# Kernel tuning notes

Hardware: AMD Instinct MI355X
Metric: run time of the kernel (lower is better)

## Reference

```python
import jax, jax.numpy as jnp
import numpy as np
from jax import lax

# Poincare ball, curvature c = 1.0 (geoopt default for CustomPoincare)
SQRT_C = 1.0
BALL_EPS = 1e-3   # projx margin (geoopt-style)
MIN_NORM = 1e-7
BN_EPS = 1e-5


def _norm(x):
    # norm over channel (last) dim, clamped away from 0
    return jnp.maximum(jnp.linalg.norm(x, axis=-1, keepdims=True), MIN_NORM)


def projx(x):
    # clip points back inside the ball of radius (1-eps)/sqrt(c)
    maxnorm = (1.0 - BALL_EPS) / SQRT_C
    n = _norm(x)
    return x * jnp.minimum(1.0, maxnorm / n)


def expmap0(v):
    # exp map at the origin: tanh(sqrt(c)||v||) * v / (sqrt(c)||v||)
    n = _norm(v)
    return projx(jnp.tanh(SQRT_C * n) * v / (SQRT_C * n))


def logmap0(x):
    # log map at the origin: artanh(sqrt(c)||x||) * x / (sqrt(c)||x||)
    n = _norm(x)
    t = jnp.minimum(SQRT_C * n, 1.0 - 1e-5)
    return jnp.arctanh(t) * x / (SQRT_C * n)


def setup_inputs() -> dict:
    key = jax.random.key(0)
    k0, k1 = jax.random.split(key)
    B, C_in, H, W, C_out = 16, 3, 224, 224, 64
    x = jax.random.normal(k0, (B, C_in, H, W), dtype=jnp.float32)
    # Kaiming-ish init for the 3x3 stem conv, HWIO layout
    fan_in = 3 * 3 * C_in
    conv_w = jax.random.normal(k1, (3, 3, C_in, C_out), dtype=jnp.float32) * np.float32(np.sqrt(2.0 / fan_in))
    conv_b = jnp.zeros((C_out,), dtype=jnp.float32)
    bn_gamma = jnp.ones((C_out,), dtype=jnp.float32)
    bn_beta = jnp.zeros((C_out,), dtype=jnp.float32)
    return {"x": x, "conv_w": conv_w, "conv_b": conv_b,
            "bn_gamma": bn_gamma, "bn_beta": bn_beta}


def reference(x, conv_w, conv_b, bn_gamma, bn_beta):
    # x: [B, C, H, W] -> NHWC (channel-last points on the Poincare ball)
    h = jnp.transpose(x, (0, 2, 3, 1))
    h = projx(h)

    # --- PoincareConv2d: tangent-space 3x3 conv (log0 -> conv+bias -> exp0) ---
    u = logmap0(h)
    u = lax.conv_general_dilated(
        u, conv_w, window_strides=(1, 1), padding="SAME",
        dimension_numbers=("NHWC", "HWIO", "NHWC"))
    u = u + conv_b
    h = expmap0(u)

    # --- PoincareBatchNorm2d: tangent-space BN over (B,H,W) per channel ---
    u = logmap0(h)
    mean = jnp.mean(u, axis=(0, 1, 2), keepdims=True)
    var = jnp.var(u, axis=(0, 1, 2), keepdims=True)
    u = (u - mean) * lax.rsqrt(var + BN_EPS) * bn_gamma + bn_beta
    h = expmap0(u)

    # --- PoincareTangentReLU ---
    h = expmap0(jax.nn.relu(logmap0(h)))
    return h  # [B, H, W, C_out]
```

## Files before the change

kernel.cpp:

```cpp
#include <hip/hip_runtime.h>
#include <math.h>

#define B_ 16
#define H_ 224
#define W_ 224
#define HP_ 226
#define WP_ 226
#define CIN_ 3
#define COUT_ 64
#define NPIX_ (B_ * H_ * W_)
#define NPAD_ (B_ * HP_ * WP_)
#define NBLK_ (NPIX_ / 256)
#define MAXNORM_ 0.999f
#define MINN_ 1e-7f
#define TCL_ (1.0f - 1e-5f)
#define LCLAMP_ 3.8002012f
#define BN_EPS_ 1e-5f
#define NF_ ((float)NPIX_)
#define PADW_ 68

typedef float v4f __attribute__((ext_vector_type(4)));

struct Acc {
  v4f v0, v1, v2, v3, v4, v5, v6, v7, v8, v9, v10, v11, v12, v13, v14, v15;
};

#define EACH16(X) X(0) X(1) X(2) X(3) X(4) X(5) X(6) X(7) \
                  X(8) X(9) X(10) X(11) X(12) X(13) X(14) X(15)

__global__ void k0_transform(const float* __restrict__ x, float4* __restrict__ u0p) {
  int idx = blockIdx.x * 256 + threadIdx.x;
  if (idx >= NPAD_) return;
  int b = idx / (HP_ * WP_);
  int r = idx % (HP_ * WP_);
  int yp = r / WP_, xp = r % WP_;
  float4 o = make_float4(0.f, 0.f, 0.f, 0.f);
  if (yp >= 1 && yp <= H_ && xp >= 1 && xp <= W_) {
    const float* xb = x + (size_t)b * (CIN_ * H_ * W_) + (size_t)(yp - 1) * W_ + (xp - 1);
    float v0 = xb[0];
    float v1 = xb[H_ * W_];
    float v2 = xb[2 * H_ * W_];
    float n = sqrtf(fmaf(v0, v0, fmaf(v1, v1, v2 * v2)));
    float ncl = fmaxf(n, MINN_);
    float s = fminf(1.0f, MAXNORM_ / ncl);
    float p0 = v0 * s, p1 = v1 * s, p2 = v2 * s;
    float np_ = fmaxf(sqrtf(fmaf(p0, p0, fmaf(p1, p1, p2 * p2))), MINN_);
    float t = fminf(np_, TCL_);
    float f = atanhf(t) / np_;
    o.x = p0 * f; o.y = p1 * f; o.z = p2 * f;
  }
  u0p[idx] = o;
}

__device__ __forceinline__ void conv_clamp(const float4* __restrict__ u0p,
                                           const float* __restrict__ wgt,
                                           const float* __restrict__ bias,
                                           int pix, Acc& a) {
  int b = pix / (H_ * W_);
  int r = pix % (H_ * W_);
  int y = r / W_, x = r % W_;
  const float4* base = u0p + ((size_t)b * HP_ + y) * WP_ + x;
  const v4f* b4 = (const v4f*)bias;
#define INIT(i) a.v##i = b4[i];
  EACH16(INIT)
#undef INIT
#define FMA_X(i) a.v##i += in.x * wp[i];
#define FMA_Y(i) a.v##i += in.y * wp[16 + i];
#define FMA_Z(i) a.v##i += in.z * wp[32 + i];
#define TAP(t) { float4 in = base[((t) / 3) * WP_ + ((t) % 3)];              \
                 const v4f* wp = (const v4f*)(wgt + (t) * 3 * COUT_);        \
                 EACH16(FMA_X) EACH16(FMA_Y) EACH16(FMA_Z) }
  TAP(0) TAP(1) TAP(2) TAP(3) TAP(4) TAP(5) TAP(6) TAP(7) TAP(8)
#undef TAP
#undef FMA_X
#undef FMA_Y
#undef FMA_Z
  v4f s2 = (v4f)0.0f;
#define SQ(i) s2 += a.v##i * a.v##i;
  EACH16(SQ)
#undef SQ
  float n2 = s2.x + s2.y + s2.z + s2.w;
  float n = sqrtf(n2);
  float sc = (n > LCLAMP_) ? (LCLAMP_ / n) : 1.0f;
#define SCL(i) a.v##i *= sc;
  EACH16(SCL)
}

__global__ void __launch_bounds__(256, 2)
k1_stats(const float4* __restrict__ u0p, const float* __restrict__ wgt,
         const float* __restrict__ bias, float* __restrict__ partials) {
  int pix = blockIdx.x * 256 + threadIdx.x;
  Acc a;
  conv_clamp(u0p, wgt, bias, pix, a);

  __shared__ __align__(16) float stg[4 * 64 * PADW_];
  __shared__ float red[512];
  int lane = threadIdx.x & 63, wid = threadIdx.x >> 6;

  float* row = stg + (size_t)(wid * 64 + lane) * PADW_;
#define STG(i) *(v4f*)(row + 4 * (i)) = a.v##i;
  EACH16(STG)
#undef STG
  __builtin_amdgcn_wave_barrier();

  const float* col = stg + (size_t)wid * 64 * PADW_ + lane;
  float s0 = 0.f, s1 = 0.f, s2 = 0.f, s3 = 0.f;
  float q0 = 0.f, q1 = 0.f, q2 = 0.f, q3 = 0.f;
#pragma unroll
  for (int p = 0; p < 64; p += 4) {
    float a0 = col[(p + 0) * PADW_];
    float a1 = col[(p + 1) * PADW_];
    float a2 = col[(p + 2) * PADW_];
    float a3 = col[(p + 3) * PADW_];
    s0 += a0; q0 = fmaf(a0, a0, q0);
    s1 += a1; q1 = fmaf(a1, a1, q1);
    s2 += a2; q2 = fmaf(a2, a2, q2);
    s3 += a3; q3 = fmaf(a3, a3, q3);
  }
  float s_tot = (s0 + s1) + (s2 + s3);
  float q_tot = (q0 + q1) + (q2 + q3);

  red[wid * 64 + lane] = s_tot;
  red[256 + wid * 64 + lane] = q_tot;
  __syncthreads();
  int tid = threadIdx.x;
  if (tid < 128) {
    int off = (tid < 64) ? 0 : (256 - 64);
    float tot = red[off + tid] + red[off + tid + 64] + red[off + tid + 128] + red[off + tid + 192];
    partials[(size_t)blockIdx.x * 128 + tid] = tot;
  }
}

__global__ void k2_finalize(const float* __restrict__ partials, const float* __restrict__ gamma,
                            float* __restrict__ stats) {
  __shared__ float lds[32 * 128 + 128];
  int tid = threadIdx.x;
  int chunk = tid >> 5, qi = tid & 31;
  const float4* p4 = (const float4*)partials;
  float4 a = make_float4(0.f, 0.f, 0.f, 0.f);
#pragma unroll 7
  for (int i = chunk; i < NBLK_; i += 32) {
    float4 v = p4[(size_t)i * 32 + qi];
    a.x += v.x; a.y += v.y; a.z += v.z; a.w += v.w;
  }
  lds[chunk * 128 + qi * 4 + 0] = a.x;
  lds[chunk * 128 + qi * 4 + 1] = a.y;
  lds[chunk * 128 + qi * 4 + 2] = a.z;
  lds[chunk * 128 + qi * 4 + 3] = a.w;
  __syncthreads();
  if (tid < 128) {
    float tot = 0.f;
#pragma unroll
    for (int ch = 0; ch < 32; ch++) tot += lds[ch * 128 + tid];
    lds[32 * 128 + tid] = tot;
  }
  __syncthreads();
  if (tid < 64) {
    float mean = lds[32 * 128 + tid] / NF_;
    float msq  = lds[32 * 128 + 64 + tid] / NF_;
    float var = msq - mean * mean;
    float rstdg = gamma[tid] / sqrtf(var + BN_EPS_);
    stats[tid] = mean;
    stats[64 + tid] = rstdg;
  }
}

__global__ void __launch_bounds__(256, 2)
k3_final(const float4* __restrict__ u0p, const float* __restrict__ wgt,
         const float* __restrict__ bias, const float* __restrict__ stats,
         const float* __restrict__ beta, float* __restrict__ out) {
  int pix = blockIdx.x * 256 + threadIdx.x;
  Acc a;
  conv_clamp(u0p, wgt, bias, pix, a);
  const v4f* mean4 = (const v4f*)stats;
  const v4f* rg4   = (const v4f*)(stats + 64);
  const v4f* beta4 = (const v4f*)beta;
  v4f s2 = (v4f)0.0f;
#define BN(i) { a.v##i = (a.v##i - mean4[i]) * rg4[i] + beta4[i]; s2 += a.v##i * a.v##i; }
  EACH16(BN)
#undef BN
  float nv2 = s2.x + s2.y + s2.z + s2.w;
  float nv = sqrtf(nv2);
  float sv = (nv > LCLAMP_) ? (LCLAMP_ / nv) : 1.0f;
  v4f z2 = (v4f)0.0f;
#define RELU(i) { v4f r = a.v##i * sv;                                      \
                  r.x = fmaxf(r.x, 0.f); r.y = fmaxf(r.y, 0.f);             \
                  r.z = fmaxf(r.z, 0.f); r.w = fmaxf(r.w, 0.f);             \
                  a.v##i = r; z2 += r * r; }
  EACH16(RELU)
#undef RELU
  float nw2 = z2.x + z2.y + z2.z + z2.w;
  float nw = fmaxf(sqrtf(nw2), MINN_);
  float th = tanhf(nw);
  float se = th / nw;
  float clip = fminf(1.0f, MAXNORM_ / fmaxf(th, MINN_));
  float fs = se * clip;

  __shared__ __align__(16) float stg[4 * 64 * PADW_];
  int lane = threadIdx.x & 63, wid = threadIdx.x >> 6;
  float* row = stg + (size_t)(wid * 64 + lane) * PADW_;
#define STG(i) *(v4f*)(row + 4 * (i)) = a.v##i * fs;
  EACH16(STG)
#undef STG
  __builtin_amdgcn_wave_barrier();

  const float* wbuf = stg + (size_t)wid * 64 * PADW_;
  v4f* outw = (v4f*)out + ((size_t)blockIdx.x * 256 + wid * 64) * 16;
  int pr = lane >> 4, ci = lane & 15;
  const float* rbase = wbuf + pr * PADW_ + ci * 4;
#pragma unroll
  for (int j = 0; j < 16; j++) {
    v4f v = *(const v4f*)(rbase + j * 4 * PADW_);
    __builtin_nontemporal_store(v, outw + j * 64 + lane);
  }
}

extern "C" void kernel_launch(void* const* d_in, const int* in_sizes, int n_in,
                              void* d_out, int out_size, void* d_ws, size_t ws_size,
                              hipStream_t stream) {
  const float* x     = (const float*)d_in[0];
  const float* wgt   = (const float*)d_in[1];
  const float* bias  = (const float*)d_in[2];
  const float* gamma = (const float*)d_in[3];
  const float* beta  = (const float*)d_in[4];
  float* out = (float*)d_out;

  char* ws = (char*)d_ws;
  float4* u0p      = (float4*)ws;
  float*  partials = (float*)(ws + (size_t)NPAD_ * 16);
  float*  stats    = (float*)(ws + (size_t)NPAD_ * 16 + (size_t)NBLK_ * 128 * 4);

  hipLaunchKernelGGL(k0_transform, dim3((NPAD_ + 255) / 256), dim3(256), 0, stream, x, u0p);
  hipLaunchKernelGGL(k1_stats,     dim3(NBLK_),               dim3(256), 0, stream, u0p, wgt, bias, partials);
  hipLaunchKernelGGL(k2_finalize,  dim3(1),                   dim3(1024), 0, stream, partials, gamma, stats);
  hipLaunchKernelGGL(k3_final,     dim3(NBLK_),               dim3(256), 0, stream, u0p, wgt, bias, stats, beta, out);
}
```

Before: 318.7 us.

## Halve LDS staging to raise occupancy, parallelize BN finalize, use fast math intrinsics

The per-wave LDS staging buffer is halved by staging the 64 channels in two 32-channel passes, and launch bounds are raised from 2 to 4 blocks per CU in the conv-stats and final kernels so more waves can hide latency. The finalize kernel now runs 64 blocks, one per channel, instead of a single 1024-thread block. The precise atanhf and tanhf calls are replaced with __logf, __expf and __fdividef forms. The higher occupancy target may force register spills given the 64-float accumulator, and the fast intrinsics slightly reduce accuracy.

After: 307.9 us. -3.4%, faster.

```diff
diff --git a/kernel.cpp b/kernel.cpp
--- a/kernel.cpp
+++ b/kernel.cpp
@@ -17,7 +17,7 @@
 #define LCLAMP_ 3.8002012f
 #define BN_EPS_ 1e-5f
 #define NF_ ((float)NPIX_)
-#define PADW_ 68
+#define PADW2_ 36
 
 typedef float v4f __attribute__((ext_vector_type(4)));
 
@@ -27,6 +27,8 @@
 
 #define EACH16(X) X(0) X(1) X(2) X(3) X(4) X(5) X(6) X(7) \
                   X(8) X(9) X(10) X(11) X(12) X(13) X(14) X(15)
+#define EACH8LO(X) X(0) X(1) X(2) X(3) X(4) X(5) X(6) X(7)
+#define EACH8HI(X) X(8) X(9) X(10) X(11) X(12) X(13) X(14) X(15)
 
 __global__ void k0_transform(const float* __restrict__ x, float4* __restrict__ u0p) {
   int idx = blockIdx.x * 256 + threadIdx.x;
@@ -46,7 +48,8 @@
     float p0 = v0 * s, p1 = v1 * s, p2 = v2 * s;
     float np_ = fmaxf(sqrtf(fmaf(p0, p0, fmaf(p1, p1, p2 * p2))), MINN_);
     float t = fminf(np_, TCL_);
-    float f = atanhf(t) / np_;
+    float ath = 0.5f * __logf(__fdividef(1.0f + t, 1.0f - t));
+    float f = __fdividef(ath, np_);
     o.x = p0 * f; o.y = p1 * f; o.z = p2 * f;
   }
   u0p[idx] = o;
@@ -86,86 +89,94 @@
   EACH16(SCL)
 }
 
-__global__ void __launch_bounds__(256, 2)
+__global__ void __launch_bounds__(256, 4)
 k1_stats(const float4* __restrict__ u0p, const float* __restrict__ wgt,
          const float* __restrict__ bias, float* __restrict__ partials) {
   int pix = blockIdx.x * 256 + threadIdx.x;
   Acc a;
   conv_clamp(u0p, wgt, bias, pix, a);
 
-  __shared__ __align__(16) float stg[4 * 64 * PADW_];
+  __shared__ __align__(16) float stg[4 * 64 * PADW2_];
   __shared__ float red[512];
   int lane = threadIdx.x & 63, wid = threadIdx.x >> 6;
-
-  float* row = stg + (size_t)(wid * 64 + lane) * PADW_;
-#define STG(i) *(v4f*)(row + 4 * (i)) = a.v##i;
-  EACH16(STG)
-#undef STG
-  __builtin_amdgcn_wave_barrier();
-
-  const float* col = stg + (size_t)wid * 64 * PADW_ + lane;
-  float s0 = 0.f, s1 = 0.f, s2 = 0.f, s3 = 0.f;
-  float q0 = 0.f, q1 = 0.f, q2 = 0.f, q3 = 0.f;
-#pragma unroll
-  for (int p = 0; p < 64; p += 4) {
-    float a0 = col[(p + 0) * PADW_];
-    float a1 = col[(p + 1) * PADW_];
-    float a2 = col[(p + 2) * PADW_];
-    float a3 = col[(p + 3) * PADW_];
-    s0 += a0; q0 = fmaf(a0, a0, q0);
-    s1 += a1; q1 = fmaf(a1, a1, q1);
-    s2 += a2; q2 = fmaf(a2, a2, q2);
-    s3 += a3; q3 = fmaf(a3, a3, q3);
-  }
-  float s_tot = (s0 + s1) + (s2 + s3);
-  float q_tot = (q0 + q1) + (q2 + q3);
-
-  red[wid * 64 + lane] = s_tot;
-  red[256 + wid * 64 + lane] = q_tot;
+  float* row = stg + (size_t)(wid * 64 + lane) * PADW2_;
+  int c = lane & 31, half = lane >> 5;
+  const float* col = stg + ((size_t)wid * 64 + half * 32) * PADW2_ + c;
+
+#define STGA(i) *(v4f*)(row + 4 * (i)) = a.v##i;
+  EACH8LO(STGA)
+#undef STGA
+  __builtin_amdgcn_wave_barrier();
+  float sA0 = 0.f, sA1 = 0.f, qA0 = 0.f, qA1 = 0.f;
+#pragma unroll
+  for (int p = 0; p < 32; p += 2) {
+    float a0 = col[(p + 0) * PADW2_];
+    float a1 = col[(p + 1) * PADW2_];
+    sA0 += a0; qA0 = fmaf(a0, a0, qA0);
+    sA1 += a1; qA1 = fmaf(a1, a1, qA1);
+  }
+  float sA = sA0 + sA1, qA = qA0 + qA1;
+  __builtin_amdgcn_wave_barrier();
+
+#define STGB(i) *(v4f*)(row + 4 * ((i) - 8)) = a.v##i;
+  EACH8HI(STGB)
+#undef STGB
+  __builtin_amdgcn_wave_barrier();
+  float sB0 = 0.f, sB1 = 0.f, qB0 = 0.f, qB1 = 0.f;
+#pragma unroll
+  for (int p = 0; p < 32; p += 2) {
+    float a0 = col[(p + 0) * PADW2_];
+    float a1 = col[(p + 1) * PADW2_];
+    sB0 += a0; qB0 = fmaf(a0, a0, qB0);
+    sB1 += a1; qB1 = fmaf(a1, a1, qB1);
+  }
+  float sB = sB0 + sB1, qB = qB0 + qB1;
+
+  sA += __shfl_xor(sA, 32, 64);  qA += __shfl_xor(qA, 32, 64);
+  sB += __shfl_xor(sB, 32, 64);  qB += __shfl_xor(qB, 32, 64);
+
+  if (lane < 32) {
+    red[0 * 128 + wid * 32 + c] = sA;
+    red[1 * 128 + wid * 32 + c] = sB;
+    red[2 * 128 + wid * 32 + c] = qA;
+    red[3 * 128 + wid * 32 + c] = qB;
+  }
   __syncthreads();
   int tid = threadIdx.x;
   if (tid < 128) {
-    int off = (tid < 64) ? 0 : (256 - 64);
-    float tot = red[off + tid] + red[off + tid + 64] + red[off + tid + 128] + red[off + tid + 192];
+    int base = (tid >> 5) * 128 + (tid & 31);
+    float tot = red[base] + red[base + 32] + red[base + 64] + red[base + 96];
     partials[(size_t)blockIdx.x * 128 + tid] = tot;
   }
 }
 
 __global__ void k2_finalize(const float* __restrict__ partials, const float* __restrict__ gamma,
                             float* __restrict__ stats) {
-  __shared__ float lds[32 * 128 + 128];
-  int tid = threadIdx.x;
-  int chunk = tid >> 5, qi = tid & 31;
-  const float4* p4 = (const float4*)partials;
-  float4 a = make_float4(0.f, 0.f, 0.f, 0.f);
-#pragma unroll 7
-  for (int i = chunk; i < NBLK_; i += 32) {
-    float4 v = p4[(size_t)i * 32 + qi];
-    a.x += v.x; a.y += v.y; a.z += v.z; a.w += v.w;
-  }
-  lds[chunk * 128 + qi * 4 + 0] = a.x;
-  lds[chunk * 128 + qi * 4 + 1] = a.y;
-  lds[chunk * 128 + qi * 4 + 2] = a.z;
-  lds[chunk * 128 + qi * 4 + 3] = a.w;
+  int c = blockIdx.x;
+  int t = threadIdx.x;
+  float s = 0.f, q = 0.f;
+  for (int i = t; i < NBLK_; i += 256) {
+    s += partials[(size_t)i * 128 + c];
+    q += partials[(size_t)i * 128 + 64 + c];
+  }
+  __shared__ float ls[256], lq[256];
+  ls[t] = s; lq[t] = q;
   __syncthreads();
-  if (tid < 128) {
-    float tot = 0.f;
-#pragma unroll
-    for (int ch = 0; ch < 32; ch++) tot += lds[ch * 128 + tid];
-    lds[32 * 128 + tid] = tot;
-  }
-  __syncthreads();
-  if (tid < 64) {
-    float mean = lds[32 * 128 + tid] / NF_;
-    float msq  = lds[32 * 128 + 64 + tid] / NF_;
+#pragma unroll
+  for (int off = 128; off > 0; off >>= 1) {
+    if (t < off) { ls[t] += ls[t + off]; lq[t] += lq[t + off]; }
+    __syncthreads();
+  }
+  if (t == 0) {
+    float mean = ls[0] / NF_;
+    float msq  = lq[0] / NF_;
     float var = msq - mean * mean;
-    float rstdg = gamma[tid] / sqrtf(var + BN_EPS_);
-    stats[tid] = mean;
-    stats[64 + tid] = rstdg;
-  }
-}
-
-__global__ void __launch_bounds__(256, 2)
+    stats[c] = mean;
+    stats[64 + c] = gamma[c] / sqrtf(var + BN_EPS_);
+  }
+}
+
+__global__ void __launch_bounds__(256, 4)
 k3_final(const float4* __restrict__ u0p, const float* __restrict__ wgt,
          const float* __restrict__ bias, const float* __restrict__ stats,
          const float* __restrict__ beta, float* __restrict__ out) {
@@ -191,27 +202,38 @@
 #undef RELU
   float nw2 = z2.x + z2.y + z2.z + z2.w;
   float nw = fmaxf(sqrtf(nw2), MINN_);
-  float th = tanhf(nw);
-  float se = th / nw;
+  float e2 = __expf(2.0f * nw);
+  float th = 1.0f - __fdividef(2.0f, e2 + 1.0f);
+  float se = __fdividef(th, nw);
   float clip = fminf(1.0f, MAXNORM_ / fmaxf(th, MINN_));
   float fs = se * clip;
 
-  __shared__ __align__(16) float stg[4 * 64 * PADW_];
+  __shared__ __align__(16) float stg[4 * 64 * PADW2_];
   int lane = threadIdx.x & 63, wid = threadIdx.x >> 6;
-  float* row = stg + (size_t)(wid * 64 + lane) * PADW_;
-#define STG(i) *(v4f*)(row + 4 * (i)) = a.v##i * fs;
-  EACH16(STG)
-#undef STG
-  __builtin_amdgcn_wave_barrier();
-
-  const float* wbuf = stg + (size_t)wid * 64 * PADW_;
+  float* row = stg + (size_t)(wid * 64 + lane) * PADW2_;
+  int pr8 = lane >> 3, qi = lane & 7;
+  const float* rb = stg + (size_t)wid * 64 * PADW2_ + pr8 * PADW2_ + qi * 4;
   v4f* outw = (v4f*)out + ((size_t)blockIdx.x * 256 + wid * 64) * 16;
-  int pr = lane >> 4, ci = lane & 15;
-  const float* rbase = wbuf + pr * PADW_ + ci * 4;
-#pragma unroll
-  for (int j = 0; j < 16; j++) {
-    v4f v = *(const v4f*)(rbase + j * 4 * PADW_);
-    __builtin_nontemporal_store(v, outw + j * 64 + lane);
+
+#define STGA(i) *(v4f*)(row + 4 * (i)) = a.v##i * fs;
+  EACH8LO(STGA)
+#undef STGA
+  __builtin_amdgcn_wave_barrier();
+#pragma unroll
+  for (int j = 0; j < 8; j++) {
+    v4f v = *(const v4f*)(rb + j * 8 * PADW2_);
+    __builtin_nontemporal_store(v, outw + (j * 8 + pr8) * 16 + qi);
+  }
+  __builtin_amdgcn_wave_barrier();
+
+#define STGB(i) *(v4f*)(row + 4 * ((i) - 8)) = a.v##i * fs;
+  EACH8HI(STGB)
+#undef STGB
+  __builtin_amdgcn_wave_barrier();
+#pragma unroll
+  for (int j = 0; j < 8; j++) {
+    v4f v = *(const v4f*)(rb + j * 8 * PADW2_);
+    __builtin_nontemporal_store(v, outw + (j * 8 + pr8) * 16 + 8 + qi);
   }
 }
 
@@ -232,6 +254,6 @@
 
   hipLaunchKernelGGL(k0_transform, dim3((NPAD_ + 255) / 256), dim3(256), 0, stream, x, u0p);
   hipLaunchKernelGGL(k1_stats,     dim3(NBLK_),               dim3(256), 0, stream, u0p, wgt, bias, partials);
-  hipLaunchKernelGGL(k2_finalize,  dim3(1),                   dim3(1024), 0, stream, partials, gamma, stats);
+  hipLaunchKernelGGL(k2_finalize,  dim3(64),                  dim3(256), 0, stream, partials, gamma, stats);
   hipLaunchKernelGGL(k3_final,     dim3(NBLK_),               dim3(256), 0, stream, u0p, wgt, bias, stats, beta, out);
 }
```
